# Optimization experiments

Hardware: AMD Instinct MI355X
Metric: run time of the kernel (lower is better)

## Reference

```python
import jax, jax.numpy as jnp
import numpy as np

BETA = 0.25

def setup_inputs() -> dict:
    key = jax.random.key(0)
    k1, k2 = jax.random.split(key)
    z_e = jax.random.normal(k1, (32768, 256), dtype=jnp.float32)
    codebook = jax.random.normal(k2, (8192, 256), dtype=jnp.float32)
    return {"z_e": z_e, "codebook": codebook}

def reference(z_e, codebook):
    # Squared distances via ||a||^2 - 2 a.b + ||b||^2 (argmin is invariant to sqrt)
    z_sq = jnp.sum(z_e * z_e, axis=1, keepdims=True)           # (B, 1)
    e_sq = jnp.sum(codebook * codebook, axis=1)                 # (K,)
    cross = jnp.einsum('bd,kd->bk', z_e, codebook)              # (B, K) GEMM
    d2 = z_sq - 2.0 * cross + e_sq[None, :]                     # (B, K)
    indices = jnp.argmin(d2, axis=1)                            # (B,)
    z_q = codebook[indices]                                     # (B, D)
    codebook_loss = jnp.mean((z_q - z_e) ** 2)
    commitment_loss = jnp.mean((z_e - z_q) ** 2)
    vq_loss = codebook_loss + BETA * commitment_loss
    # straight-through value (grad semantics irrelevant in fwd-only)
    z_q_st = z_e + (z_q - z_e)
    return (z_q_st, indices, vq_loss)
```

## Files before the change

### kernel.cpp

```cpp
#include <hip/hip_runtime.h>
#include <hip/hip_bf16.h>
#include <stdint.h>

#define M_ROWS 32768
#define N_CODES 8192
#define K_DIM 256
#define NSLICE 32
#define MARGIN 0.25f
#define MAXCAND 2560

#define BM 256
#define BN 256

typedef _Float16 half8 __attribute__((ext_vector_type(8)));
typedef float f4v __attribute__((ext_vector_type(4)));
typedef float f32x4 __attribute__((ext_vector_type(4)));
typedef __attribute__((address_space(3))) void lds_void;
typedef const __attribute__((address_space(1))) void gbl_cvoid;

__device__ __forceinline__ unsigned mono32(float f) {
    unsigned u = __float_as_uint(f);
    return (u & 0x80000000u) ? ~u : (u | 0x80000000u);
}
__device__ __forceinline__ unsigned long long pack_key(float d, unsigned col) {
    return ((unsigned long long)mono32(d) << 32) | (unsigned long long)col;
}
__device__ __forceinline__ float unpack_key(unsigned long long k) {
    unsigned m = (unsigned)(k >> 32);
    unsigned u = (m & 0x80000000u) ? (m & 0x7fffffffu) : ~m;
    return __uint_as_float(u);
}
__device__ __forceinline__ void merge2(unsigned long long& b1, unsigned long long& b2,
                                       unsigned long long o1, unsigned long long o2) {
    unsigned long long n1 = b1 < o1 ? b1 : o1;
    unsigned long long hi = b1 < o1 ? o1 : b1;
    unsigned long long l2 = b2 < o2 ? b2 : o2;
    b2 = hi < l2 ? hi : l2;
    b1 = n1;
}

__global__ __launch_bounds__(256) void prep_all(const float* __restrict__ z,
                                                const float* __restrict__ cb,
                                                _Float16* __restrict__ Aq,
                                                _Float16* __restrict__ Bq,
                                                float* __restrict__ esq) {
    int b = blockIdx.x;
    if (b < 5120) {
        const float* src = (b < 4096) ? z : cb;
        _Float16* dst = (b < 4096) ? Aq : Bq;
        int e = (b < 4096 ? b : b - 4096) * 256 + threadIdx.x;
        int ln = e & 63, kcg = (e >> 6) & 7, R = e >> 9;
        int row = R * 16 + (ln & 15);
        int k = kcg * 32 + (ln >> 4) * 8;
        const f4v* s4 = (const f4v*)(src + (size_t)row * K_DIM + k);
        f4v v0 = s4[0], v1 = s4[1];
        half8 h;
        #pragma unroll
        for (int j = 0; j < 4; ++j) h[j] = (_Float16)v0[j];
        #pragma unroll
        for (int j = 0; j < 4; ++j) h[4 + j] = (_Float16)v1[j];
        *(half8*)(dst + (size_t)e * 8) = h;
    } else {
        int wave = threadIdx.x >> 6, lane = threadIdx.x & 63;
        int row = (b - 5120) * 4 + wave;
        f4v v = *(const f4v*)(cb + (size_t)row * K_DIM + lane * 4);
        float sq = v[0] * v[0] + v[1] * v[1] + v[2] * v[2] + v[3] * v[3];
        #pragma unroll
        for (int m = 32; m; m >>= 1) sq += __shfl_xor(sq, m);
        if (lane == 0) esq[row] = sq;
    }
}

__global__ __launch_bounds__(512, 2) void coarse_gemm(
        const _Float16* __restrict__ Aq, const _Float16* __restrict__ Bq,
        const float* __restrict__ esq, ulonglong2* __restrict__ slices) {
    __shared__ __align__(16) char smem[131072];
    uint2 (*red)[2] = (uint2(*)[2])smem;

    int bid = blockIdx.x;
    int bn = bid & 31;
    int bm = bid >> 5;
    int m0 = bm * BM, n0 = bn * BN;

    int t = threadIdx.x;
    int lane = t & 63, wave = t >> 6;
    int l15 = lane & 15, quad = lane >> 4;
    int wr = wave >> 1, wc = wave & 1;

    float es_adj[8];
    #pragma unroll
    for (int ni = 0; ni < 8; ++ni)
        es_adj[ni] = esq[n0 + wc * 128 + ni * 16 + l15] + 1024.0f;
    asm volatile("" ::: "memory");

    f32x4 acc[4][8] = {};

    const char* Ab = (const char*)Aq + (size_t)bm * 131072;
    const char* Bb = (const char*)Bq + (size_t)bn * 131072;

    auto stage = [&](int ks, int buf) {
        char* As = smem + buf * 32768;
        char* Bs = As + 16384;
        #pragma unroll
        for (int i = 0; i < 2; ++i) {
            int e = i * 512 + t;
            int RB = e >> 6, ln = e & 63;
            size_t goff = ((size_t)(RB * 8 + ks) << 10) + (size_t)ln * 16;
            __builtin_amdgcn_global_load_lds((gbl_cvoid*)(Ab + goff),
                                             (lds_void*)(As + e * 16), 16, 0, 0);
            __builtin_amdgcn_global_load_lds((gbl_cvoid*)(Bb + goff),
                                             (lds_void*)(Bs + e * 16), 16, 0, 0);
        }
    };

    stage(0, 0);
    stage(1, 1);

    half8 a[4], b[8];
    auto body = [&](int ks, bool do_stage) {
        __builtin_amdgcn_s_barrier();
        asm volatile("" ::: "memory");
        const char* As = smem + (ks & 3) * 32768;
        const char* Bs = As + 16384;
        #pragma unroll
        for (int mi = 0; mi < 4; ++mi)
            a[mi] = *(const half8*)(As + ((wr * 4 + mi) * 64 + lane) * 16);
        #pragma unroll
        for (int ni = 0; ni < 8; ++ni)
            b[ni] = *(const half8*)(Bs + ((wc * 8 + ni) * 64 + lane) * 16);
        if (do_stage) stage(ks + 2, (ks + 2) & 3);
        __builtin_amdgcn_s_setprio(1);
        #pragma unroll
        for (int mi = 0; mi < 4; ++mi)
            #pragma unroll
            for (int ni = 0; ni < 8; ++ni)
                acc[mi][ni] = __builtin_amdgcn_mfma_f32_16x16x32_f16(
                    a[mi], b[ni], acc[mi][ni], 0, 0, 0);
        __builtin_amdgcn_s_setprio(0);
    };

    asm volatile("s_waitcnt vmcnt(4)" ::: "memory"); body(0, true);
    asm volatile("s_waitcnt vmcnt(4)" ::: "memory"); body(1, true);
    asm volatile("s_waitcnt vmcnt(4)" ::: "memory"); body(2, true);
    asm volatile("s_waitcnt vmcnt(4)" ::: "memory"); body(3, true);
    asm volatile("s_waitcnt vmcnt(4)" ::: "memory"); body(4, true);
    asm volatile("s_waitcnt vmcnt(4)" ::: "memory"); body(5, true);
    asm volatile("s_waitcnt vmcnt(4)" ::: "memory"); body(6, false);
    asm volatile("s_waitcnt vmcnt(0)" ::: "memory"); body(7, false);

    #pragma unroll
    for (int mi = 0; mi < 4; ++mi) {
        #pragma unroll
        for (int r = 0; r < 4; ++r) {
            unsigned b1 = 0xFFFFFFFFu, b2 = 0xFFFFFFFFu;
            #pragma unroll
            for (int ni = 0; ni < 8; ++ni) {
                float key = fmaf(-2.0f, acc[mi][ni][r], es_adj[ni]);
                unsigned kb = (__float_as_uint(key) & 0xFFFFFF80u) |
                              (unsigned)(ni * 16 + l15);
                unsigned hi = kb > b1 ? kb : b1;
                b1 = kb < b1 ? kb : b1;
                b2 = hi < b2 ? hi : b2;
            }
            #pragma unroll
            for (int m = 1; m < 16; m <<= 1) {
                unsigned o1 = (unsigned)__shfl_xor((int)b1, m);
                unsigned o2 = (unsigned)__shfl_xor((int)b2, m);
                unsigned hi = b1 > o1 ? b1 : o1;
                b1 = b1 < o1 ? b1 : o1;
                unsigned l2 = b2 < o2 ? b2 : o2;
                b2 = hi < l2 ? hi : l2;
            }
            if (l15 == 0) {
                int rowl = wr * 64 + mi * 16 + quad * 4 + r;
                red[rowl][wc] = make_uint2(b1, b2);
            }
        }
    }
    __syncthreads();
    if (t < 256) {
        uint2 p0 = red[t][0], p1 = red[t][1];
        unsigned m1 = p0.x < p1.x ? p0.x : p1.x;
        unsigned hi = p0.x < p1.x ? p1.x : p0.x;
        unsigned sel = p1.x < p0.x ? 1u : 0u;
        unsigned l2 = p0.y < p1.y ? p0.y : p1.y;
        unsigned m2 = hi < l2 ? hi : l2;
        unsigned col = (unsigned)n0 + sel * 128u + (m1 & 127u);
        unsigned long long q1 =
            ((unsigned long long)((m1 & 0xFFFFFF80u) | 0x80000000u) << 32) | col;
        unsigned long long q2 =
            ((unsigned long long)((m2 & 0xFFFFFF80u) | 0x80000000u) << 32) |
            0xFFFFFFFFull;
        slices[(size_t)(m0 + t) * NSLICE + bn] = make_ulonglong2(q1, q2);
    }
}

__global__ __launch_bounds__(256) void merge_slices(
        const ulonglong2* __restrict__ slices,
        int* __restrict__ bestidx, int* __restrict__ flags,
        int* __restrict__ list, int* __restrict__ count) {
    int t = threadIdx.x;
    int wave = t >> 6, lane = t & 63;
    int half = lane >> 5, idx = lane & 31;
    int row = blockIdx.x * 8 + wave * 2 + half;
    ulonglong2 p = slices[(size_t)row * NSLICE + idx];
    unsigned long long b1 = p.x, b2 = p.y;
    #pragma unroll
    for (int m = 1; m < 32; m <<= 1) {
        unsigned long long o1 = (unsigned long long)__shfl_xor((long long)b1, m);
        unsigned long long o2 = (unsigned long long)__shfl_xor((long long)b2, m);
        merge2(b1, b2, o1, o2);
    }
    if (idx == 0) {
        bestidx[row] = (int)(unsigned)(b1 & 0xFFFFFFFFULL);
        int f = (unpack_key(b2) - unpack_key(b1) <= MARGIN) ? 1 : 0;
        flags[row] = f;
        if (f) { int pos = atomicAdd(count, 1); list[pos] = row; }
    }
}

__global__ __launch_bounds__(256) void refine(
        const float* __restrict__ z, const float* __restrict__ cb,
        const ulonglong2* __restrict__ slices,
        const int* __restrict__ list, const int* __restrict__ count,
        int* __restrict__ bestidx) {
    __shared__ float zrow[K_DIM];
    __shared__ int cand[MAXCAND];
    __shared__ int ncand_s;
    __shared__ unsigned long long sb1;
    __shared__ double wd[4];
    __shared__ int wc[4];
    int t = threadIdx.x, lane = t & 63, wave = t >> 6;
    int n = *count;
    #pragma unroll 1
    for (int li = blockIdx.x; li < n; li += 2048) {
        int row = list[li];
        __syncthreads();
        zrow[t] = z[(size_t)row * K_DIM + t];
        if (t == 0) ncand_s = 0;
        __syncthreads();
        ulonglong2 p = make_ulonglong2(~0ULL, ~0ULL);
        if (wave == 0) {
            if (lane < NSLICE) p = slices[(size_t)row * NSLICE + lane];
            unsigned long long b1 = p.x;
            #pragma unroll
            for (int m = 1; m < 64; m <<= 1) {
                unsigned long long o =
                    (unsigned long long)__shfl_xor((long long)b1, m);
                b1 = o < b1 ? o : b1;
            }
            if (lane == 0) sb1 = b1;
        }
        __syncthreads();
        float thr = unpack_key(sb1) + MARGIN;
        if (wave == 0 && lane < NSLICE) {
            float k1 = unpack_key(p.x), k2 = unpack_key(p.y);
            if (k2 <= thr) {
                int pos = atomicAdd(&ncand_s, 256);
                if (pos + 256 <= MAXCAND)
                    for (int j = 0; j < 256; ++j) cand[pos + j] = lane * 256 + j;
            } else if (k1 <= thr) {
                int pos = atomicAdd(&ncand_s, 1);
                if (pos < MAXCAND) cand[pos] = (int)(unsigned)(p.x & 0xFFFFFFFFULL);
            }
        }
        __syncthreads();
        int nc = ncand_s;
        bool full = nc > MAXCAND;
        int total = full ? N_CODES : nc;
        double bd = 1e300;
        int bc = 0x7fffffff;
        #pragma unroll 1
        for (int base = 0; base < total; base += 256) {
            int i = base + t;
            if (i < total) {
                int code = full ? i : cand[i];
                const f4v* e4 = (const f4v*)(cb + (size_t)code * K_DIM);
                double s0 = 0, s1 = 0, s2 = 0, s3 = 0;
                #pragma unroll 4
                for (int k4 = 0; k4 < 64; ++k4) {
                    f4v e = e4[k4];
                    f4v zz = *(const f4v*)&zrow[k4 * 4];
                    float d0 = zz[0] - e[0], d1 = zz[1] - e[1];
                    float d2 = zz[2] - e[2], d3 = zz[3] - e[3];
                    s0 = fma((double)d0, (double)d0, s0);
                    s1 = fma((double)d1, (double)d1, s1);
                    s2 = fma((double)d2, (double)d2, s2);
                    s3 = fma((double)d3, (double)d3, s3);
                }
                double s = (s0 + s1) + (s2 + s3);
                if (s < bd || (s == bd && code < bc)) { bd = s; bc = code; }
            }
        }
        #pragma unroll
        for (int m = 1; m < 64; m <<= 1) {
            double od = __shfl_xor(bd, m);
            int oc = __shfl_xor(bc, m);
            if (od < bd || (od == bd && oc < bc)) { bd = od; bc = oc; }
        }
        if (lane == 0) { wd[wave] = bd; wc[wave] = bc; }
        __syncthreads();
        if (t == 0) {
            #pragma unroll
            for (int w = 1; w < 4; ++w)
                if (wd[w] < bd || (wd[w] == bd && wc[w] < bc)) { bd = wd[w]; bc = wc[w]; }
            bestidx[row] = bc;
        }
    }
}

__global__ __launch_bounds__(256) void vq_bruteforce(const float* __restrict__ z,
                                                     const float* __restrict__ cb,
                                                     float* __restrict__ out_idx) {
    __shared__ float As[128 * 16];
    __shared__ float Bs[128 * 16];
    int t = threadIdx.x;
    int tx = t & 15, ty = t >> 4;
    int r0 = blockIdx.x * 128;
    unsigned long long best[8];
    #pragma unroll
    for (int j = 0; j < 8; ++j) best[j] = ~0ULL;

    for (int n0 = 0; n0 < N_CODES; n0 += 128) {
        float acc[8][8] = {};
        for (int k0 = 0; k0 < K_DIM; k0 += 16) {
            __syncthreads();
            int row = t >> 1, c8 = (t & 1) * 8;
            #pragma unroll
            for (int j = 0; j < 8; ++j)
                As[row * 16 + c8 + j] = z[(size_t)(r0 + row) * K_DIM + k0 + c8 + j];
            #pragma unroll
            for (int j = 0; j < 8; ++j)
                Bs[row * 16 + c8 + j] = cb[(size_t)(n0 + row) * K_DIM + k0 + c8 + j];
            __syncthreads();
            #pragma unroll
            for (int k = 0; k < 16; ++k) {
                float a[8], b[8];
                #pragma unroll
                for (int j = 0; j < 8; ++j) a[j] = As[(ty * 8 + j) * 16 + k];
                #pragma unroll
                for (int j = 0; j < 8; ++j) b[j] = Bs[(tx * 8 + j) * 16 + k];
                #pragma unroll
                for (int i = 0; i < 8; ++i)
                    #pragma unroll
                    for (int j = 0; j < 8; ++j) {
                        float d = a[i] - b[j];
                        acc[i][j] += d * d;
                    }
            }
        }
        #pragma unroll
        for (int i = 0; i < 8; ++i) {
            unsigned long long bv = ~0ULL;
            #pragma unroll
            for (int j = 0; j < 8; ++j) {
                unsigned long long p =
                    pack_key(acc[i][j], (unsigned)(n0 + tx * 8 + j));
                bv = (p < bv) ? p : bv;
            }
            #pragma unroll
            for (int m = 1; m < 16; m <<= 1) {
                unsigned long long o =
                    (unsigned long long)__shfl_xor((long long)bv, m);
                bv = (o < bv) ? o : bv;
            }
            if (tx == 0 && bv < best[i]) best[i] = bv;
        }
    }
    if (tx == 0) {
        #pragma unroll
        for (int i = 0; i < 8; ++i)
            out_idx[r0 + ty * 8 + i] =
                (float)(unsigned)(best[i] & 0xFFFFFFFFULL);
    }
}

__global__ __launch_bounds__(256) void finalize(const float* __restrict__ z,
                                                const float* __restrict__ cb,
                                                const int* __restrict__ bestidx,
                                                float* __restrict__ out,
                                                double* __restrict__ accum,
                                                int use_int) {
    int wave = threadIdx.x >> 6, lane = threadIdx.x & 63;
    float* out_idx = out + (size_t)M_ROWS * K_DIM;
    float se = 0.f;
    #pragma unroll 1
    for (int row = blockIdx.x * 4 + wave; row < M_ROWS; row += 1024 * 4) {
        int idx = use_int ? bestidx[row] : (int)out_idx[row];
        f4v zv = *(const f4v*)(z  + (size_t)row * K_DIM + lane * 4);
        f4v qv = *(const f4v*)(cb + (size_t)idx * K_DIM + lane * 4);
        f4v ov;
        #pragma unroll
        for (int j = 0; j < 4; ++j) {
            float d = qv[j] - zv[j];
            ov[j] = zv[j] + d;
            se += d * d;
        }
        *(f4v*)(out + (size_t)row * K_DIM + lane * 4) = ov;
        if (lane == 0) out_idx[row] = (float)idx;
    }
    #pragma unroll
    for (int m = 32; m; m >>= 1) se += __shfl_xor(se, m);
    __shared__ float part[4];
    if (lane == 0) part[wave] = se;
    __syncthreads();
    if (threadIdx.x == 0)
        atomicAdd(accum, (double)((part[0] + part[1]) + (part[2] + part[3])));
}

__global__ void write_loss(const double* __restrict__ accum,
                           float* __restrict__ out) {
    out[(size_t)M_ROWS * K_DIM + M_ROWS] =
        (float)(1.25 * (*accum / (double)((size_t)M_ROWS * K_DIM)));
}

extern "C" void kernel_launch(void* const* d_in, const int* in_sizes, int n_in,
                              void* d_out, int out_size, void* d_ws, size_t ws_size,
                              hipStream_t stream) {
    const float* z  = (const float*)d_in[0];
    const float* cb = (const float*)d_in[1];
    float* out = (float*)d_out;
    float* out_idx = out + (size_t)M_ROWS * K_DIM;

    size_t offA  = 0;
    size_t offBq = offA + (size_t)M_ROWS * K_DIM * 2;
    size_t offE  = offBq + (size_t)N_CODES * K_DIM * 2;
    size_t offS  = offE + (size_t)N_CODES * 4;
    size_t offBI = offS + (size_t)M_ROWS * NSLICE * 16;
    size_t offF  = offBI + (size_t)M_ROWS * 4;
    size_t offL  = offF + (size_t)M_ROWS * 4;
    size_t offC  = offL + (size_t)M_ROWS * 4;
    size_t offAcc = offC + 16;
    size_t need  = offAcc + 16;

    if (ws_size >= need) {
        _Float16* Aq = (_Float16*)((char*)d_ws + offA);
        _Float16* Bq = (_Float16*)((char*)d_ws + offBq);
        float* esq   = (float*)((char*)d_ws + offE);
        ulonglong2* slices = (ulonglong2*)((char*)d_ws + offS);
        int* bestidx = (int*)((char*)d_ws + offBI);
        int* flags   = (int*)((char*)d_ws + offF);
        int* list    = (int*)((char*)d_ws + offL);
        int* count   = (int*)((char*)d_ws + offC);
        double* accum = (double*)((char*)d_ws + offAcc);

        hipMemsetAsync((char*)d_ws + offC, 0, 32, stream);

        prep_all<<<7168, 256, 0, stream>>>(z, cb, Aq, Bq, esq);
        coarse_gemm<<<(M_ROWS / BM) * (N_CODES / BN), 512, 0, stream>>>(
            Aq, Bq, esq, slices);
        merge_slices<<<M_ROWS / 8, 256, 0, stream>>>(slices, bestidx, flags,
                                                     list, count);
        refine<<<2048, 256, 0, stream>>>(z, cb, slices, list, count, bestidx);
        finalize<<<1024, 256, 0, stream>>>(z, cb, bestidx, out, accum, 1);
        write_loss<<<1, 1, 0, stream>>>(accum, out);
    } else {
        double* accum = (double*)d_ws;
        hipMemsetAsync(d_ws, 0, sizeof(double), stream);
        vq_bruteforce<<<M_ROWS / 128, 256, 0, stream>>>(z, cb, out_idx);
        finalize<<<1024, 256, 0, stream>>>(z, cb, nullptr, out, accum, 0);
        write_loss<<<1, 1, 0, stream>>>(accum, out);
    }
}
```

Before: 342.2 us.

## Shrink coarse GEMM N-tile to 128 with double-buffered pipeline and 64 slices

Halves the coarse GEMM column tile from 256 to 128 codes, cuts LDS from 128KB to 48KB and raises the launch-bounds occupancy hint from 2 to 4 blocks. The 4-deep buffered pipeline with manual vmcnt waits and setprio is replaced by a plain double-buffered loop with __syncthreads. The per-row slice count doubles to 64, so merge_slices and refine are updated to handle 64 slices of 128 codes each. The intent is better latency hiding through more resident blocks, at the cost of lower per-block data reuse, twice as much slice traffic, and a simpler pipeline.

```diff
diff --git a/kernel.cpp b/kernel.cpp
--- a/kernel.cpp
+++ b/kernel.cpp
@@ -5,12 +5,12 @@
 #define M_ROWS 32768
 #define N_CODES 8192
 #define K_DIM 256
-#define NSLICE 32
+#define NSLICE 64
 #define MARGIN 0.25f
 #define MAXCAND 2560
 
 #define BM 256
-#define BN 256
+#define BN 128
 
 typedef _Float16 half8 __attribute__((ext_vector_type(8)));
 typedef float f4v __attribute__((ext_vector_type(4)));
@@ -71,15 +71,15 @@
     }
 }
 
-__global__ __launch_bounds__(512, 2) void coarse_gemm(
+__global__ __launch_bounds__(512, 4) void coarse_gemm(
         const _Float16* __restrict__ Aq, const _Float16* __restrict__ Bq,
         const float* __restrict__ esq, ulonglong2* __restrict__ slices) {
-    __shared__ __align__(16) char smem[131072];
+    __shared__ __align__(16) char smem[49152];
     uint2 (*red)[2] = (uint2(*)[2])smem;
 
     int bid = blockIdx.x;
-    int bn = bid & 31;
-    int bm = bid >> 5;
+    int bn = bid & 63;
+    int bm = bid >> 6;
     int m0 = bm * BM, n0 = bn * BN;
 
     int t = threadIdx.x;
@@ -87,19 +87,18 @@
     int l15 = lane & 15, quad = lane >> 4;
     int wr = wave >> 1, wc = wave & 1;
 
-    float es_adj[8];
-    #pragma unroll
-    for (int ni = 0; ni < 8; ++ni)
-        es_adj[ni] = esq[n0 + wc * 128 + ni * 16 + l15] + 1024.0f;
-    asm volatile("" ::: "memory");
-
-    f32x4 acc[4][8] = {};
+    float es_adj[4];
+    #pragma unroll
+    for (int ni = 0; ni < 4; ++ni)
+        es_adj[ni] = esq[n0 + wc * 64 + ni * 16 + l15] + 1024.0f;
+
+    f32x4 acc[4][4] = {};
 
     const char* Ab = (const char*)Aq + (size_t)bm * 131072;
-    const char* Bb = (const char*)Bq + (size_t)bn * 131072;
+    const char* Bb = (const char*)Bq + (size_t)bn * 65536;
 
     auto stage = [&](int ks, int buf) {
-        char* As = smem + buf * 32768;
+        char* As = smem + buf * 24576;
         char* Bs = As + 16384;
         #pragma unroll
         for (int i = 0; i < 2; ++i) {
@@ -108,45 +107,41 @@
             size_t goff = ((size_t)(RB * 8 + ks) << 10) + (size_t)ln * 16;
             __builtin_amdgcn_global_load_lds((gbl_cvoid*)(Ab + goff),
                                              (lds_void*)(As + e * 16), 16, 0, 0);
+        }
+        {
+            int CB = t >> 6, ln = t & 63;
+            size_t goff = ((size_t)(CB * 8 + ks) << 10) + (size_t)ln * 16;
             __builtin_amdgcn_global_load_lds((gbl_cvoid*)(Bb + goff),
-                                             (lds_void*)(Bs + e * 16), 16, 0, 0);
+                                             (lds_void*)(Bs + t * 16), 16, 0, 0);
         }
     };
 
-    stage(0, 0);
-    stage(1, 1);
-
-    half8 a[4], b[8];
-    auto body = [&](int ks, bool do_stage) {
-        __builtin_amdgcn_s_barrier();
-        asm volatile("" ::: "memory");
-        const char* As = smem + (ks & 3) * 32768;
+    auto compute = [&](int buf) {
+        const char* As = smem + buf * 24576;
         const char* Bs = As + 16384;
+        half8 a[4], b[4];
         #pragma unroll
         for (int mi = 0; mi < 4; ++mi)
             a[mi] = *(const half8*)(As + ((wr * 4 + mi) * 64 + lane) * 16);
         #pragma unroll
-        for (int ni = 0; ni < 8; ++ni)
-            b[ni] = *(const half8*)(Bs + ((wc * 8 + ni) * 64 + lane) * 16);
-        if (do_stage) stage(ks + 2, (ks + 2) & 3);
-        __builtin_amdgcn_s_setprio(1);
+        for (int ni = 0; ni < 4; ++ni)
+            b[ni] = *(const half8*)(Bs + ((wc * 4 + ni) * 64 + lane) * 16);
         #pragma unroll
         for (int mi = 0; mi < 4; ++mi)
             #pragma unroll
-            for (int ni = 0; ni < 8; ++ni)
+            for (int ni = 0; ni < 4; ++ni)
                 acc[mi][ni] = __builtin_amdgcn_mfma_f32_16x16x32_f16(
                     a[mi], b[ni], acc[mi][ni], 0, 0, 0);
-        __builtin_amdgcn_s_setprio(0);
     };
 
-    asm volatile("s_waitcnt vmcnt(4)" ::: "memory"); body(0, true);
-    asm volatile("s_waitcnt vmcnt(4)" ::: "memory"); body(1, true);
-    asm volatile("s_waitcnt vmcnt(4)" ::: "memory"); body(2, true);
-    asm volatile("s_waitcnt vmcnt(4)" ::: "memory"); body(3, true);
-    asm volatile("s_waitcnt vmcnt(4)" ::: "memory"); body(4, true);
-    asm volatile("s_waitcnt vmcnt(4)" ::: "memory"); body(5, true);
-    asm volatile("s_waitcnt vmcnt(4)" ::: "memory"); body(6, false);
-    asm volatile("s_waitcnt vmcnt(0)" ::: "memory"); body(7, false);
+    stage(0, 0);
+    __syncthreads();
+    #pragma unroll
+    for (int ks = 0; ks < 8; ++ks) {
+        if (ks < 7) stage(ks + 1, (ks + 1) & 1);
+        compute(ks & 1);
+        __syncthreads();
+    }
 
     #pragma unroll
     for (int mi = 0; mi < 4; ++mi) {
@@ -154,10 +149,10 @@
         for (int r = 0; r < 4; ++r) {
             unsigned b1 = 0xFFFFFFFFu, b2 = 0xFFFFFFFFu;
             #pragma unroll
-            for (int ni = 0; ni < 8; ++ni) {
+            for (int ni = 0; ni < 4; ++ni) {
                 float key = fmaf(-2.0f, acc[mi][ni][r], es_adj[ni]);
                 unsigned kb = (__float_as_uint(key) & 0xFFFFFF80u) |
-                              (unsigned)(ni * 16 + l15);
+                              (unsigned)(wc * 64 + ni * 16 + l15);
                 unsigned hi = kb > b1 ? kb : b1;
                 b1 = kb < b1 ? kb : b1;
                 b2 = hi < b2 ? hi : b2;
@@ -182,10 +177,9 @@
         uint2 p0 = red[t][0], p1 = red[t][1];
         unsigned m1 = p0.x < p1.x ? p0.x : p1.x;
         unsigned hi = p0.x < p1.x ? p1.x : p0.x;
-        unsigned sel = p1.x < p0.x ? 1u : 0u;
         unsigned l2 = p0.y < p1.y ? p0.y : p1.y;
         unsigned m2 = hi < l2 ? hi : l2;
-        unsigned col = (unsigned)n0 + sel * 128u + (m1 & 127u);
+        unsigned col = (unsigned)n0 + (m1 & 127u);
         unsigned long long q1 =
             ((unsigned long long)((m1 & 0xFFFFFF80u) | 0x80000000u) << 32) | col;
         unsigned long long q2 =
@@ -199,19 +193,17 @@
         const ulonglong2* __restrict__ slices,
         int* __restrict__ bestidx, int* __restrict__ flags,
         int* __restrict__ list, int* __restrict__ count) {
-    int t = threadIdx.x;
-    int wave = t >> 6, lane = t & 63;
-    int half = lane >> 5, idx = lane & 31;
-    int row = blockIdx.x * 8 + wave * 2 + half;
-    ulonglong2 p = slices[(size_t)row * NSLICE + idx];
+    int wave = threadIdx.x >> 6, lane = threadIdx.x & 63;
+    int row = blockIdx.x * 4 + wave;
+    ulonglong2 p = slices[(size_t)row * NSLICE + lane];
     unsigned long long b1 = p.x, b2 = p.y;
     #pragma unroll
-    for (int m = 1; m < 32; m <<= 1) {
+    for (int m = 1; m < 64; m <<= 1) {
         unsigned long long o1 = (unsigned long long)__shfl_xor((long long)b1, m);
         unsigned long long o2 = (unsigned long long)__shfl_xor((long long)b2, m);
         merge2(b1, b2, o1, o2);
     }
-    if (idx == 0) {
+    if (lane == 0) {
         bestidx[row] = (int)(unsigned)(b1 & 0xFFFFFFFFULL);
         int f = (unpack_key(b2) - unpack_key(b1) <= MARGIN) ? 1 : 0;
         flags[row] = f;
@@ -241,7 +233,7 @@
         __syncthreads();
         ulonglong2 p = make_ulonglong2(~0ULL, ~0ULL);
         if (wave == 0) {
-            if (lane < NSLICE) p = slices[(size_t)row * NSLICE + lane];
+            p = slices[(size_t)row * NSLICE + lane];
             unsigned long long b1 = p.x;
             #pragma unroll
             for (int m = 1; m < 64; m <<= 1) {
@@ -253,12 +245,12 @@
         }
         __syncthreads();
         float thr = unpack_key(sb1) + MARGIN;
-        if (wave == 0 && lane < NSLICE) {
+        if (wave == 0) {
             float k1 = unpack_key(p.x), k2 = unpack_key(p.y);
             if (k2 <= thr) {
-                int pos = atomicAdd(&ncand_s, 256);
-                if (pos + 256 <= MAXCAND)
-                    for (int j = 0; j < 256; ++j) cand[pos + j] = lane * 256 + j;
+                int pos = atomicAdd(&ncand_s, 128);
+                if (pos + 128 <= MAXCAND)
+                    for (int j = 0; j < 128; ++j) cand[pos + j] = lane * 128 + j;
             } else if (k1 <= thr) {
                 int pos = atomicAdd(&ncand_s, 1);
                 if (pos < MAXCAND) cand[pos] = (int)(unsigned)(p.x & 0xFFFFFFFFULL);
@@ -449,7 +441,7 @@
         prep_all<<<7168, 256, 0, stream>>>(z, cb, Aq, Bq, esq);
         coarse_gemm<<<(M_ROWS / BM) * (N_CODES / BN), 512, 0, stream>>>(
             Aq, Bq, esq, slices);
-        merge_slices<<<M_ROWS / 8, 256, 0, stream>>>(slices, bestidx, flags,
+        merge_slices<<<M_ROWS / 4, 256, 0, stream>>>(slices, bestidx, flags,
                                                      list, count);
         refine<<<2048, 256, 0, stream>>>(z, cb, slices, list, count, bestidx);
         finalize<<<1024, 256, 0, stream>>>(z, cb, bestidx, out, accum, 1);
```

After: 364.2 us. 6.4% more time.

## Restructure coarse GEMM into 2x4 wave grid with half-K ping-pong staging

Applied to the files above, without the earlier changes.

The coarse fp16 GEMM changes its wave layout from 4x2 to 2x4, so each wave now computes 128 rows by 64 codes. The K loop becomes 4 big chunks double-buffered in 64KB LDS halves, and each chunk is split into sub-steps whose global-to-LDS loads interleave with MFMA groups. Extra barriers, sched_barrier and lgkmcnt waits are added to overlap loads with compute more finely. The top-2 reduction now merges four column groups with a 6-bit index field, which slightly coarsens key precision and adds more barrier synchronisation.

```diff
diff --git a/kernel.cpp b/kernel.cpp
--- a/kernel.cpp
+++ b/kernel.cpp
@@ -75,7 +75,7 @@
         const _Float16* __restrict__ Aq, const _Float16* __restrict__ Bq,
         const float* __restrict__ esq, ulonglong2* __restrict__ slices) {
     __shared__ __align__(16) char smem[131072];
-    uint2 (*red)[2] = (uint2(*)[2])smem;
+    uint2 (*red)[4] = (uint2(*)[4])smem;
 
     int bid = blockIdx.x;
     int bn = bid & 31;
@@ -85,78 +85,96 @@
     int t = threadIdx.x;
     int lane = t & 63, wave = t >> 6;
     int l15 = lane & 15, quad = lane >> 4;
-    int wr = wave >> 1, wc = wave & 1;
-
-    float es_adj[8];
-    #pragma unroll
-    for (int ni = 0; ni < 8; ++ni)
-        es_adj[ni] = esq[n0 + wc * 128 + ni * 16 + l15] + 1024.0f;
+    int wr = wave >> 2, wc = wave & 3;
+
+    float es_adj[4];
+    #pragma unroll
+    for (int ni = 0; ni < 4; ++ni)
+        es_adj[ni] = esq[n0 + wc * 64 + ni * 16 + l15] + 1024.0f;
     asm volatile("" ::: "memory");
 
-    f32x4 acc[4][8] = {};
+    f32x4 acc[8][4] = {};
 
     const char* Ab = (const char*)Aq + (size_t)bm * 131072;
     const char* Bb = (const char*)Bq + (size_t)bn * 131072;
 
-    auto stage = [&](int ks, int buf) {
-        char* As = smem + buf * 32768;
-        char* Bs = As + 16384;
-        #pragma unroll
-        for (int i = 0; i < 2; ++i) {
-            int e = i * 512 + t;
+    auto stage_half = [&](int ks, int op, int c, char* dstA, char* dstB) {
+        const char* gb = op ? Bb : Ab;
+        char* db = op ? dstB : dstA;
+        #pragma unroll
+        for (int i2 = 0; i2 < 2; ++i2) {
+            int e = i2 * 512 + t;
             int RB = e >> 6, ln = e & 63;
-            size_t goff = ((size_t)(RB * 8 + ks) << 10) + (size_t)ln * 16;
-            __builtin_amdgcn_global_load_lds((gbl_cvoid*)(Ab + goff),
-                                             (lds_void*)(As + e * 16), 16, 0, 0);
-            __builtin_amdgcn_global_load_lds((gbl_cvoid*)(Bb + goff),
-                                             (lds_void*)(Bs + e * 16), 16, 0, 0);
+            __builtin_amdgcn_global_load_lds(
+                (gbl_cvoid*)(gb + ((size_t)(RB * 8 + ks * 2 + c) << 10) + ln * 16),
+                (lds_void*)(db + ((RB * 2 + c) * 64 + ln) * 16), 16, 0, 0);
         }
     };
 
-    stage(0, 0);
-    stage(1, 1);
-
-    half8 a[4], b[8];
-    auto body = [&](int ks, bool do_stage) {
-        __builtin_amdgcn_s_barrier();
-        asm volatile("" ::: "memory");
-        const char* As = smem + (ks & 3) * 32768;
-        const char* Bs = As + 16384;
-        #pragma unroll
-        for (int mi = 0; mi < 4; ++mi)
-            a[mi] = *(const half8*)(As + ((wr * 4 + mi) * 64 + lane) * 16);
-        #pragma unroll
-        for (int ni = 0; ni < 8; ++ni)
-            b[ni] = *(const half8*)(Bs + ((wc * 8 + ni) * 64 + lane) * 16);
-        if (do_stage) stage(ks + 2, (ks + 2) & 3);
-        __builtin_amdgcn_s_setprio(1);
-        #pragma unroll
-        for (int mi = 0; mi < 4; ++mi)
-            #pragma unroll
-            for (int ni = 0; ni < 8; ++ni)
-                acc[mi][ni] = __builtin_amdgcn_mfma_f32_16x16x32_f16(
-                    a[mi], b[ni], acc[mi][ni], 0, 0, 0);
-        __builtin_amdgcn_s_setprio(0);
-    };
-
-    asm volatile("s_waitcnt vmcnt(4)" ::: "memory"); body(0, true);
-    asm volatile("s_waitcnt vmcnt(4)" ::: "memory"); body(1, true);
-    asm volatile("s_waitcnt vmcnt(4)" ::: "memory"); body(2, true);
-    asm volatile("s_waitcnt vmcnt(4)" ::: "memory"); body(3, true);
-    asm volatile("s_waitcnt vmcnt(4)" ::: "memory"); body(4, true);
-    asm volatile("s_waitcnt vmcnt(4)" ::: "memory"); body(5, true);
-    asm volatile("s_waitcnt vmcnt(4)" ::: "memory"); body(6, false);
-    asm volatile("s_waitcnt vmcnt(0)" ::: "memory"); body(7, false);
-
-    #pragma unroll
-    for (int mi = 0; mi < 4; ++mi) {
+    {
+        char* A0 = smem, * B0 = smem + 32768;
+        stage_half(0, 0, 0, A0, B0);
+        stage_half(0, 1, 0, A0, B0);
+        stage_half(0, 0, 1, A0, B0);
+        stage_half(0, 1, 1, A0, B0);
+    }
+
+    half8 bfr[4];
+    #pragma unroll
+    for (int j = 0; j < 4; ++j) {
+        const char* As = smem + (j & 1) * 65536;
+        const char* Bs = As + 32768;
+        char* Asn = smem + ((j + 1) & 1) * 65536;
+        char* Bsn = Asn + 32768;
+        #pragma unroll
+        for (int p = 0; p < 4; ++p) {
+            const int c = p >> 1;
+            const int mh = p & 1;
+            if (p == 0 || p == 2) {
+                if (j == 3 && p == 2)
+                    asm volatile("s_waitcnt vmcnt(0)" ::: "memory");
+                else
+                    asm volatile("s_waitcnt vmcnt(4)" ::: "memory");
+                __builtin_amdgcn_s_barrier();
+                asm volatile("" ::: "memory");
+            }
+            half8 afr[4];
+            #pragma unroll
+            for (int mi = 0; mi < 4; ++mi) {
+                int RB = wr * 8 + mh * 4 + mi;
+                afr[mi] = *(const half8*)(As + ((RB * 2 + c) * 64 + lane) * 16);
+            }
+            if (mh == 0) {
+                #pragma unroll
+                for (int ni = 0; ni < 4; ++ni) {
+                    int CB = wc * 4 + ni;
+                    bfr[ni] = *(const half8*)(Bs + ((CB * 2 + c) * 64 + lane) * 16);
+                }
+            }
+            if (j < 3) stage_half(j + 1, p & 1, p >> 1, Asn, Bsn);
+            __builtin_amdgcn_s_barrier();
+            asm volatile("s_waitcnt lgkmcnt(0)" ::: "memory");
+            __builtin_amdgcn_sched_barrier(0);
+            __builtin_amdgcn_s_setprio(1);
+            #pragma unroll
+            for (int mi = 0; mi < 4; ++mi)
+                #pragma unroll
+                for (int ni = 0; ni < 4; ++ni)
+                    acc[mh * 4 + mi][ni] = __builtin_amdgcn_mfma_f32_16x16x32_f16(
+                        afr[mi], bfr[ni], acc[mh * 4 + mi][ni], 0, 0, 0);
+            __builtin_amdgcn_s_setprio(0);
+        }
+    }
+
+    #pragma unroll
+    for (int mi = 0; mi < 8; ++mi) {
         #pragma unroll
         for (int r = 0; r < 4; ++r) {
             unsigned b1 = 0xFFFFFFFFu, b2 = 0xFFFFFFFFu;
             #pragma unroll
-            for (int ni = 0; ni < 8; ++ni) {
+            for (int ni = 0; ni < 4; ++ni) {
                 float key = fmaf(-2.0f, acc[mi][ni][r], es_adj[ni]);
-                unsigned kb = (__float_as_uint(key) & 0xFFFFFF80u) |
+                unsigned kb = (__float_as_uint(key) & 0xFFFFFFC0u) |
                               (unsigned)(ni * 16 + l15);
                 unsigned hi = kb > b1 ? kb : b1;
                 b1 = kb < b1 ? kb : b1;
@@ -172,24 +190,26 @@
                 b2 = hi < l2 ? hi : l2;
             }
             if (l15 == 0) {
-                int rowl = wr * 64 + mi * 16 + quad * 4 + r;
+                int rowl = wr * 128 + mi * 16 + quad * 4 + r;
                 red[rowl][wc] = make_uint2(b1, b2);
             }
         }
     }
     __syncthreads();
     if (t < 256) {
-        uint2 p0 = red[t][0], p1 = red[t][1];
-        unsigned m1 = p0.x < p1.x ? p0.x : p1.x;
-        unsigned hi = p0.x < p1.x ? p1.x : p0.x;
-        unsigned sel = p1.x < p0.x ? 1u : 0u;
-        unsigned l2 = p0.y < p1.y ? p0.y : p1.y;
-        unsigned m2 = hi < l2 ? hi : l2;
-        unsigned col = (unsigned)n0 + sel * 128u + (m1 & 127u);
+        unsigned best = 0xFFFFFFFFu, sec = 0xFFFFFFFFu, bq = 0;
+        #pragma unroll
+        for (int q = 0; q < 4; ++q) {
+            uint2 e = red[t][q];
+            if (e.x < best) { sec = best; best = e.x; bq = (unsigned)q; }
+            else sec = e.x < sec ? e.x : sec;
+            sec = e.y < sec ? e.y : sec;
+        }
+        unsigned col = (unsigned)n0 + bq * 64u + (best & 63u);
         unsigned long long q1 =
-            ((unsigned long long)((m1 & 0xFFFFFF80u) | 0x80000000u) << 32) | col;
+            ((unsigned long long)((best & 0xFFFFFFC0u) | 0x80000000u) << 32) | col;
         unsigned long long q2 =
-            ((unsigned long long)((m2 & 0xFFFFFF80u) | 0x80000000u) << 32) |
+            ((unsigned long long)((sec & 0xFFFFFFC0u) | 0x80000000u) << 32) |
             0xFFFFFFFFull;
         slices[(size_t)(m0 + t) * NSLICE + bn] = make_ulonglong2(q1, q2);
     }
```

Result: slower. 391.3 us (+14.4%).
